# Performance work log

Measured on AMD Instinct MI355X. Metric: run time of the kernel, lower is better.

## Reference

```python
import jax, jax.numpy as jnp
import numpy as np

B, O, OBS, A, H = 512, 16, 128, 4, 64 * 8  # H=512
H = 512
LN_EPS = 1e-5


def _lin_init(key, fan_in, fan_out):
    k1, k2 = jax.random.split(key)
    lim = 1.0 / np.sqrt(fan_in)
    W = jax.random.uniform(k1, (fan_in, fan_out), jnp.float32, -lim, lim)
    b = jax.random.uniform(k2, (fan_out,), jnp.float32, -lim, lim)
    return W, b


def setup_inputs() -> dict:
    key = jax.random.key(0)
    ks = jax.random.split(key, 10)
    states = jax.random.normal(ks[0], (B, O, OBS), jnp.float32)
    action = jax.random.randint(ks[1], (B,), 0, A * O, jnp.int64)
    eW1, eb1 = _lin_init(ks[2], 2 * OBS, H)
    eW2, eb2 = _lin_init(ks[3], H, H)
    eW3, eb3 = _lin_init(ks[4], H, H)
    nW1, nb1 = _lin_init(ks[5], H + OBS + A, H)
    nW2, nb2 = _lin_init(ks[6], H, H)
    nW3, nb3 = _lin_init(ks[7], H, OBS)
    return dict(states=states, action=action,
                eW1=eW1, eb1=eb1, eW2=eW2, eb2=eb2,
                eg=jnp.ones((H,), jnp.float32), ebeta=jnp.zeros((H,), jnp.float32),
                eW3=eW3, eb3=eb3,
                nW1=nW1, nb1=nb1, nW2=nW2, nb2=nb2,
                ng=jnp.ones((H,), jnp.float32), nbeta=jnp.zeros((H,), jnp.float32),
                nW3=nW3, nb3=nb3)


def _ln(x, g, b):
    mu = jnp.mean(x, axis=-1, keepdims=True)
    var = jnp.mean((x - mu) ** 2, axis=-1, keepdims=True)
    return (x - mu) * jax.lax.rsqrt(var + LN_EPS) * g + b


def _mlp(x, W1, b1, W2, b2, g, beta, W3, b3):
    h = jax.nn.relu(x @ W1 + b1)
    h = jax.nn.relu(_ln(h @ W2 + b2, g, beta))
    return h @ W3 + b3


def _edge_index():
    # torch nonzero order: (i, j) for i in range(O), j != i; then batch offsets
    i = jnp.arange(O)[:, None]                   # [O,1]
    k = jnp.arange(O - 1)[None, :]               # [1,O-1]
    j = k + (k >= i)                             # skip self-loop
    row_l = jnp.broadcast_to(i, (O, O - 1)).reshape(-1)
    col_l = j.reshape(-1)
    off = (jnp.arange(B) * O)[:, None]           # [B,1]
    row = (row_l[None, :] + off).reshape(-1)     # [B*O*(O-1)]
    col = (col_l[None, :] + off).reshape(-1)
    return row, col


def reference(states, action, eW1, eb1, eW2, eb2, eg, ebeta, eW3, eb3,
              nW1, nb1, nW2, nb2, ng, nbeta, nW3, nb3):
    nodes = states.reshape(B * O, OBS)
    row, col = _edge_index()
    # edge model: gather pairs -> MLP
    e_in = jnp.concatenate([nodes[row], nodes[col]], axis=1)    # [E, 2*OBS]
    edge_attr = _mlp(e_in, eW1, eb1, eW2, eb2, eg, ebeta, eW3, eb3)  # [E, H]
    # action: one-hot over A*O, reshaped per-node
    act_vec = jax.nn.one_hot(action, A * O, dtype=states.dtype).reshape(B * O, A)
    node_in = jnp.concatenate([nodes, act_vec], axis=1)         # [B*O, OBS+A]
    # scatter: unsorted segment sum over source index (row)
    agg = jax.ops.segment_sum(edge_attr, row, num_segments=B * O)  # [B*O, H]
    node_in = jnp.concatenate([node_in, agg], axis=1)           # [B*O, OBS+A+H]
    out = _mlp(node_in, nW1, nb1, nW2, nb2, ng, nbeta, nW3, nb3)
    return out.reshape(B, O, OBS)
```

## Files before the change

kernel.cpp:

```cpp
#include <hip/hip_runtime.h>
#include <hip/hip_bf16.h>


using bf16 = __hip_bfloat16;
typedef __attribute__((ext_vector_type(8))) short bf16x8;
typedef __attribute__((ext_vector_type(4))) short short4v;
typedef __attribute__((ext_vector_type(4))) float f32x4;

#define LDK 40
#define LDQ 1032
#define LDN 520
#define LDT 72

#define SEG_EW1 32768
#define SEG_EW2 65536
#define SEG_EW3 65536
#define SEG_NW1 82432
#define SEG_NW2 65536
#define SEG_NW3 16384
#define SEG_EB3 128
#define SEG_NB1 128
#define SEG_TOT (SEG_EW1+SEG_EW2+SEG_EW3+SEG_NW1+SEG_NW2+SEG_NW3+SEG_EB3+SEG_NB1)

__device__ int g_valid = 0;
__device__ __align__(16) float g_wcopy[SEG_TOT * 4];
__device__ __align__(16) short g_eW1f[131072];
__device__ __align__(16) short g_eW2f[262144];
__device__ __align__(16) short g_nW1nf[65536];
__device__ __align__(16) short g_nW2f[262144];
__device__ __align__(16) short g_nW3f[65536];
__device__ __align__(16) short g_Wcf[262144];
__device__ __align__(16) float g_bfold[512];

__device__ __forceinline__ short f2bf(float f) {
  bf16 h = __float2bfloat16(f);
  return *reinterpret_cast<short*>(&h);
}
__device__ __forceinline__ float bs2f(short s) {
  bf16 h = *reinterpret_cast<bf16*>(&s);
  return __bfloat162float(h);
}
__device__ __forceinline__ f32x4 mfma16(bf16x8 a, bf16x8 b, f32x4 c) {
  return __builtin_amdgcn_mfma_f32_16x16x32_bf16(a, b, c, 0, 0, 0);
}
__device__ __forceinline__ bf16x8 ld8f(const float* p) {
  float4 a = *(const float4*)p;
  float4 b = *(const float4*)(p + 4);
  bf16x8 o;
  o[0] = f2bf(a.x); o[1] = f2bf(a.y); o[2] = f2bf(a.z); o[3] = f2bf(a.w);
  o[4] = f2bf(b.x); o[5] = f2bf(b.y); o[6] = f2bf(b.z); o[7] = f2bf(b.w);
  return o;
}
__device__ __forceinline__ void lgkm0_barrier() {
  asm volatile("s_waitcnt lgkmcnt(0)" ::: "memory");
  __builtin_amdgcn_s_barrier();
  asm volatile("" ::: "memory");
}

__global__ __launch_bounds__(256) void wcheck(
    const float* __restrict__ eW1, const float* __restrict__ eW2,
    const float* __restrict__ eW3, const float* __restrict__ nW1,
    const float* __restrict__ nW2, const float* __restrict__ nW3,
    const float* __restrict__ eb3, const float* __restrict__ nb1) {
  const int nt = gridDim.x * 256;
  const int tid = blockIdx.x * 256 + threadIdx.x;
  bool dirty = false;
#pragma unroll
  for (int k = 0; k < 4; ++k) {
    int idx = k * nt + tid;
    if (idx >= SEG_TOT) break;
    int i = idx;
    const uint4* src;
    if (i < SEG_EW1) src = (const uint4*)eW1 + i;
    else if ((i -= SEG_EW1) < SEG_EW2) src = (const uint4*)eW2 + i;
    else if ((i -= SEG_EW2) < SEG_EW3) src = (const uint4*)eW3 + i;
    else if ((i -= SEG_EW3) < SEG_NW1) src = (const uint4*)nW1 + i;
    else if ((i -= SEG_NW1) < SEG_NW2) src = (const uint4*)nW2 + i;
    else if ((i -= SEG_NW2) < SEG_NW3) src = (const uint4*)nW3 + i;
    else if ((i -= SEG_NW3) < SEG_EB3) src = (const uint4*)eb3 + i;
    else { i -= SEG_EB3; src = (const uint4*)nb1 + i; }
    uint4 a = *src;
    uint4* cp = (uint4*)g_wcopy + idx;
    uint4 b = *cp;
    if (a.x != b.x || a.y != b.y || a.z != b.z || a.w != b.w) {
      *cp = a;
      dirty = true;
    }
  }
  if (dirty) g_valid = 0;
}

__global__ __launch_bounds__(256) void mega_prep(
    const float* __restrict__ eW3, short* __restrict__ eW3b,
    const float* __restrict__ nW1, unsigned short* __restrict__ nW1at,
    const float* __restrict__ eW1, const float* __restrict__ eW2,
    const float* __restrict__ nW2, const float* __restrict__ nW3) {
  if (g_valid) return;
  __shared__ unsigned short ttile[32][33];
  __shared__ short ftile[32 * LDT];
  const int z = blockIdx.z, bx = blockIdx.x, t = threadIdx.x;
  if (z == 0) {
    if (bx >= 256) return;
    int i = (bx * 256 + t) * 4;
    float4 v = *(const float4*)(eW3 + i);
    short4v o;
    o.x = f2bf(v.x); o.y = f2bf(v.y); o.z = f2bf(v.z); o.w = f2bf(v.w);
    *(short4v*)(eW3b + i) = o;
    return;
  }
  if (z == 1) {
    if (bx >= 256) return;
    const float* src = nW1 + 132 * 512;
    int bc = (bx & 15) * 32, br = (bx >> 4) * 32;
    int tx = t & 31, ty = t >> 5;
    for (int i = ty; i < 32; i += 8) {
      short s = f2bf(src[(size_t)(br + i) * 512 + bc + tx]);
      ttile[i][tx] = *reinterpret_cast<unsigned short*>(&s);
    }
    __syncthreads();
    for (int i = ty; i < 32; i += 8)
      nW1at[(size_t)(bc + i) * 512 + br + tx] = ttile[tx][i];
    return;
  }
  const float* W;
  short* out;
  int ldw, kts, gq, goff, tot_sh;
  switch (z) {
    case 2: W = eW1;           out = g_eW1f;  ldw = 512; kts = 4;  gq = 8; goff = 0;  tot_sh = 6; break;
    case 3: W = eW1 + 128*512; out = g_eW1f;  ldw = 512; kts = 4;  gq = 8; goff = 32; tot_sh = 6; break;
    case 4: W = eW2;           out = g_eW2f;  ldw = 512; kts = 16; gq = 8; goff = 0;  tot_sh = 5; break;
    case 5: W = nW1;           out = g_nW1nf; ldw = 512; kts = 4;  gq = 8; goff = 0;  tot_sh = 5; break;
    case 6: W = nW2;           out = g_nW2f;  ldw = 512; kts = 16; gq = 8; goff = 0;  tot_sh = 5; break;
    default: W = nW3;          out = g_nW3f;  ldw = 128; kts = 16; gq = 2; goff = 0;  tot_sh = 3; break;
  }
  if (bx >= kts * gq) return;
  const int kt = bx / gq, qg = bx % gq;
  {
    int r = t >> 3, c0 = (t & 7) * 8;
    const float* src = W + (size_t)(kt * 32 + r) * ldw + qg * 64 + c0;
    *(bf16x8*)&ftile[r * LDT + c0] = ld8f(src);
  }
  __syncthreads();
  {
    int og = t >> 6, lane = t & 63, q = lane >> 4, lc = lane & 15;
    int gg = qg * 4 + og;
    size_t base = ((size_t)((kt << tot_sh) + gg + goff)) << 9;
    bf16x8 v;
#pragma unroll
    for (int j = 0; j < 8; ++j) v[j] = ftile[(q * 8 + j) * LDT + og * 16 + lc];
    *(bf16x8*)(out + base + lane * 8) = v;
  }
}

__global__ __launch_bounds__(256) void combo96(
    const bf16* __restrict__ nW1at, const bf16* __restrict__ eW3b,
    const float* __restrict__ eb3, const float* __restrict__ nb1,
    const float* __restrict__ nW1) {
  if (g_valid) return;
  __shared__ short Al[64 * LDK];
  __shared__ short Bl[64 * LDK];
  __shared__ float red[256];
  const int bid = blockIdx.x;
  const int t = threadIdx.x;
  const int wid = t >> 6, lane = t & 63, q = lane >> 4, lc = lane & 15;
  const f32x4 zz = {0.f, 0.f, 0.f, 0.f};

  if (bid < 64) {
    const int wm = wid >> 1, wn = wid & 1;
    const int n0 = (bid >> 3) * 64, k0 = (bid & 7) * 64;
    f32x4 acc[2][2];
#pragma unroll
    for (int mb = 0; mb < 2; ++mb)
#pragma unroll
      for (int nb = 0; nb < 2; ++nb) acc[mb][nb] = zz;
    const int sr = t >> 2, seg = t & 3;
    for (int h0 = 0; h0 < 512; h0 += 32) {
      *(uint4*)&Al[sr * LDK + seg * 8] =
          *(const uint4*)(nW1at + (size_t)(n0 + sr) * 512 + h0 + seg * 8);
      *(uint4*)&Bl[sr * LDK + seg * 8] =
          *(const uint4*)(eW3b + (size_t)(k0 + sr) * 512 + h0 + seg * 8);
      __syncthreads();
      bf16x8 af[2], bfr[2];
#pragma unroll
      for (int mb = 0; mb < 2; ++mb)
        af[mb] = *(const bf16x8*)&Al[(wm * 32 + mb * 16 + lc) * LDK + q * 8];
#pragma unroll
      for (int nb = 0; nb < 2; ++nb)
        bfr[nb] = *(const bf16x8*)&Bl[(wn * 32 + nb * 16 + lc) * LDK + q * 8];
#pragma unroll
      for (int mb = 0; mb < 2; ++mb)
#pragma unroll
        for (int nb = 0; nb < 2; ++nb)
          acc[mb][nb] = mfma16(af[mb], bfr[nb], acc[mb][nb]);
      __syncthreads();
    }
#pragma unroll
    for (int mb = 0; mb < 2; ++mb)
#pragma unroll
      for (int nb = 0; nb < 2; ++nb)
#pragma unroll
        for (int r = 0; r < 4; ++r) {
          int n = n0 + wm * 32 + mb * 16 + q * 4 + r;
          int k = k0 + wn * 32 + nb * 16 + lc;
          int kt = k >> 5, kin = k & 31, qf = kin >> 3, jf = kin & 7;
          g_Wcf[(((size_t)kt * 32 + (n >> 4)) * 64 + qf * 16 + (n & 15)) * 8 +
                jf] = f2bf(acc[mb][nb][r]);
        }
    return;
  }
  {
    const int n = (bid - 64) * 16 + (t & 15);
    const int sl = t >> 4;
    float s = 0.f;
#pragma unroll 8
    for (int h = sl * 32; h < sl * 32 + 32; ++h)
      s += eb3[h] * nW1[(size_t)(132 + h) * 512 + n];
    red[sl * 16 + (t & 15)] = s;
    __syncthreads();
    if (t < 16) {
      float tot = 0.f;
#pragma unroll
      for (int k = 0; k < 16; ++k) tot += red[k * 16 + t];
      g_bfold[(bid - 64) * 16 + t] = nb1[(bid - 64) * 16 + t] + 15.f * tot;
    }
  }
}

__global__ __launch_bounds__(512, 4) void mega(
    const float* __restrict__ states, const int* __restrict__ action,
    const float* __restrict__ eb1, const float* __restrict__ eb2,
    const float* __restrict__ eg, const float* __restrict__ ebt,
    const float* __restrict__ nW1, const float* __restrict__ nb2,
    const float* __restrict__ ng, const float* __restrict__ nbt,
    const float* __restrict__ nb3, float* __restrict__ Out) {
  __shared__ __align__(16) char smem[71168];
  short* PQL = (short*)(smem);
  short* sts = (short*)(smem + 33024);
  short* AbS = (short*)(smem + 33024);
  float* s_sum = (float*)(smem + 49408);
  float* s_sq = (float*)(smem + 51712);
  float* mr = (float*)(smem + 54016);
  short* SL = (short*)(smem + 54528);
  short* n1s = PQL;

  const bf16* const eW1f = (const bf16*)g_eW1f;
  const bf16* const eW2f = (const bf16*)g_eW2f;
  const bf16* const nW1nf = (const bf16*)g_nW1nf;
  const bf16* const nW2f = (const bf16*)g_nW2f;
  const bf16* const nW3f = (const bf16*)g_nW3f;
  const bf16* const Wcf = (const bf16*)g_Wcf;
  const float* const bfold = g_bfold;

  const int t = threadIdx.x;
  const int w = t >> 6, lane = t & 63, q = lane >> 4, lc = lane & 15;
  const int bb = blockIdx.x;

  if (bb == 0 && t == 0) g_valid = 1;

  if (t < 256) {
    int r = t >> 4, c8 = (t & 15) * 8;
    *(bf16x8*)&sts[r * 136 + c8] =
        ld8f(states + ((size_t)bb * 16 + r) * 128 + c8);
  }
  __syncthreads();

  {
    f32x4 acc[8];
#pragma unroll
    for (int nb = 0; nb < 8; ++nb) {
      int col = w * 128 + nb * 16 + lc;
      float bv = (col < 512) ? eb1[col] : 0.f;
      acc[nb] = {bv, bv, bv, bv};
    }
#pragma unroll
    for (int kt = 0; kt < 4; ++kt) {
      bf16x8 af = *(const bf16x8*)&sts[lc * 136 + kt * 32 + q * 8];
#pragma unroll
      for (int nb = 0; nb < 8; ++nb) {
        bf16x8 bfr = *(const bf16x8*)(eW1f +
                                      (((size_t)kt * 64 + w * 8 + nb) * 64 +
                                       lane) * 8);
        acc[nb] = mfma16(af, bfr, acc[nb]);
      }
    }
#pragma unroll
    for (int nb = 0; nb < 8; ++nb) {
      int col = w * 128 + nb * 16 + lc;
#pragma unroll
      for (int r = 0; r < 4; ++r)
        PQL[(q * 4 + r) * LDQ + col] = f2bf(acc[nb][r]);
    }
  }
  __syncthreads();

  const int ar = t >> 3;
  const int j8 = t & 7;
  const int gA = ar >> 4;
  const int slot = ar & 15;
  const bool padA = (slot == 15);
  const int wu = j8 ^ (ar & 7);
  const int aoff0 = lc * 64 + ((q ^ (lc & 7)) * 8);
  const int aoff1 = lc * 64 + (((4 + q) ^ (lc & 7)) * 8);
  const bf16* const eW2w = eW2f + (size_t)(w * 4) * 512 + lane * 8;
  short* const wdst0 = AbS + ar * 64 + wu * 8;

#pragma unroll 1
  for (int sg = 0; sg < 4; ++sg) {
    const int srcb = sg * 4 + gA;
    const int dstb = padA ? 0 : slot + (slot >= srcb ? 1 : 0);
    const short* pA = PQL + srcb * LDQ + j8 * 8;
    const short* qA = PQL + dstb * LDQ + 512 + j8 * 8;

    auto build = [&](int ks, int buf) {
      bf16x8 av = {0, 0, 0, 0, 0, 0, 0, 0};
      if (!padA) {
        bf16x8 pv = *(const bf16x8*)(pA + ks * 64);
        bf16x8 qv = *(const bf16x8*)(qA + ks * 64);
#pragma unroll
        for (int e = 0; e < 8; ++e)
          av[e] = f2bf(fmaxf(bs2f(pv[e]) + bs2f(qv[e]), 0.f));
      }
      *(bf16x8*)(wdst0 + buf * 4096) = av;
    };

    f32x4 acc[4][4];
#pragma unroll
    for (int nb = 0; nb < 4; ++nb) {
      float bv = eb2[w * 64 + nb * 16 + lc];
#pragma unroll
      for (int mb = 0; mb < 4; ++mb) acc[mb][nb] = {bv, bv, bv, bv};
    }

    build(0, 0);
    lgkm0_barrier();

#pragma unroll 1
    for (int ks = 0; ks < 8; ++ks) {
      const int cur = ks & 1;
      const short* Abc = AbS + cur * 4096;
      const bf16* bks = eW2w + (size_t)ks * 32768;
      bf16x8 a0[4], b0[4];
#pragma unroll
      for (int mb = 0; mb < 4; ++mb)
        a0[mb] = *(const bf16x8*)&Abc[mb * 1024 + aoff0];
#pragma unroll
      for (int nb = 0; nb < 4; ++nb)
        b0[nb] = *(const bf16x8*)(bks + nb * 512);
      __builtin_amdgcn_s_setprio(1);
#pragma unroll
      for (int mb = 0; mb < 4; ++mb)
#pragma unroll
        for (int nb = 0; nb < 4; ++nb)
          acc[mb][nb] = mfma16(a0[mb], b0[nb], acc[mb][nb]);
      __builtin_amdgcn_s_setprio(0);
      bf16x8 a1[4], b1[4];
#pragma unroll
      for (int nb = 0; nb < 4; ++nb)
        b1[nb] = *(const bf16x8*)(bks + 16384 + nb * 512);
#pragma unroll
      for (int mb = 0; mb < 4; ++mb)
        a1[mb] = *(const bf16x8*)&Abc[mb * 1024 + aoff1];
      if (ks < 7) build(ks + 1, cur ^ 1);
      __builtin_amdgcn_s_setprio(1);
#pragma unroll
      for (int mb = 0; mb < 4; ++mb)
#pragma unroll
        for (int nb = 0; nb < 4; ++nb)
          acc[mb][nb] = mfma16(a1[mb], b1[nb], acc[mb][nb]);
      __builtin_amdgcn_s_setprio(0);
      lgkm0_barrier();
    }

    float gv[4], bev[4];
#pragma unroll
    for (int nb = 0; nb < 4; ++nb) {
      int col = w * 64 + nb * 16 + lc;
      gv[nb] = eg[col];
      bev[nb] = ebt[col];
    }
#pragma unroll
    for (int mb = 0; mb < 4; ++mb) {
      float ps[4] = {0, 0, 0, 0}, pq2[4] = {0, 0, 0, 0};
#pragma unroll
      for (int nb = 0; nb < 4; ++nb)
#pragma unroll
        for (int r = 0; r < 4; ++r) {
          float x = acc[mb][nb][r];
          ps[r] += x;
          pq2[r] += x * x;
        }
#pragma unroll
      for (int d = 1; d < 16; d <<= 1)
#pragma unroll
        for (int r = 0; r < 4; ++r) {
          ps[r] += __shfl_xor(ps[r], d, 64);
          pq2[r] += __shfl_xor(pq2[r], d, 64);
        }
      if (lc == 0)
#pragma unroll
        for (int r = 0; r < 4; ++r) {
          int row = mb * 16 + q * 4 + r;
          s_sum[row * 9 + w] = ps[r];
          s_sq[row * 9 + w] = pq2[r];
        }
    }
    __syncthreads();
    if (t < 64) {
      float tot = 0.f, tsq = 0.f;
#pragma unroll
      for (int wv = 0; wv < 8; ++wv) {
        tot += s_sum[t * 9 + wv];
        tsq += s_sq[t * 9 + wv];
      }
      float m = tot * (1.f / 512.f);
      mr[t * 2] = m;
      mr[t * 2 + 1] = rsqrtf(tsq * (1.f / 512.f) - m * m + 1e-5f);
    }
    __syncthreads();
#pragma unroll
    for (int mb = 0; mb < 4; ++mb) {
      float sv[4] = {0, 0, 0, 0};
#pragma unroll
      for (int r = 0; r < 4; ++r) {
        int row = mb * 16 + q * 4 + r;
        float m = mr[row * 2], rstd = mr[row * 2 + 1];
#pragma unroll
        for (int nb = 0; nb < 4; ++nb) {
          float h = (acc[mb][nb][r] - m) * rstd * gv[nb] + bev[nb];
          h = fmaxf(h, 0.f);
          if (q * 4 + r != 15) sv[nb] += h;
        }
      }
#pragma unroll
      for (int nb = 0; nb < 4; ++nb) {
        sv[nb] += __shfl_xor(sv[nb], 16, 64);
        sv[nb] += __shfl_xor(sv[nb], 32, 64);
      }
      if (lane < 16)
#pragma unroll
        for (int nb = 0; nb < 4; ++nb)
          SL[(sg * 4 + mb) * LDN + w * 64 + nb * 16 + lc] = f2bf(sv[nb]);
    }
  }
  __syncthreads();

  if (t < 256) {
    int r = t >> 4, c8 = (t & 15) * 8;
    *(bf16x8*)&sts[r * 136 + c8] =
        ld8f(states + ((size_t)bb * 16 + r) * 128 + c8);
  }
  __syncthreads();

  {
    f32x4 acc[4];
#pragma unroll
    for (int nb = 0; nb < 4; ++nb) {
      float bv = bfold[w * 64 + nb * 16 + lc];
      acc[nb] = {bv, bv, bv, bv};
    }
#pragma unroll
    for (int kt = 0; kt < 4; ++kt) {
      bf16x8 af = *(const bf16x8*)&sts[lc * 136 + kt * 32 + q * 8];
#pragma unroll
      for (int nb = 0; nb < 4; ++nb) {
        bf16x8 bfr = *(const bf16x8*)(nW1nf +
                                      (((size_t)kt * 32 + w * 4 + nb) * 64 +
                                       lane) * 8);
        acc[nb] = mfma16(af, bfr, acc[nb]);
      }
    }
#pragma unroll 2
    for (int kt = 0; kt < 16; ++kt) {
      bf16x8 af = *(const bf16x8*)&SL[lc * LDN + kt * 32 + q * 8];
#pragma unroll
      for (int nb = 0; nb < 4; ++nb) {
        bf16x8 bfr = *(const bf16x8*)(Wcf +
                                      (((size_t)kt * 32 + w * 4 + nb) * 64 +
                                       lane) * 8);
        acc[nb] = mfma16(af, bfr, acc[nb]);
      }
    }
    int a = action[bb];
    int aw = a >> 2, ac4 = a & 3;
#pragma unroll
    for (int nb = 0; nb < 4; ++nb) {
      int col = w * 64 + nb * 16 + lc;
      float awv = nW1[(size_t)(128 + ac4) * 512 + col];
#pragma unroll
      for (int r = 0; r < 4; ++r) {
        int row = q * 4 + r;
        float x = acc[nb][r] + (row == aw ? awv : 0.f);
        n1s[row * LDN + col] = f2bf(fmaxf(x, 0.f));
      }
    }
  }
  __syncthreads();

  {
    f32x4 acc[4];
#pragma unroll
    for (int nb = 0; nb < 4; ++nb) {
      float bv = nb2[w * 64 + nb * 16 + lc];
      acc[nb] = {bv, bv, bv, bv};
    }
#pragma unroll 2
    for (int kt = 0; kt < 16; ++kt) {
      bf16x8 af = *(const bf16x8*)&n1s[lc * LDN + kt * 32 + q * 8];
#pragma unroll
      for (int nb = 0; nb < 4; ++nb) {
        bf16x8 bfr = *(const bf16x8*)(nW2f +
                                      (((size_t)kt * 32 + w * 4 + nb) * 64 +
                                       lane) * 8);
        acc[nb] = mfma16(af, bfr, acc[nb]);
      }
    }
    float gv[4], bev[4];
    float ps[4] = {0, 0, 0, 0}, pq2[4] = {0, 0, 0, 0};
#pragma unroll
    for (int nb = 0; nb < 4; ++nb) {
      int col = w * 64 + nb * 16 + lc;
      gv[nb] = ng[col];
      bev[nb] = nbt[col];
#pragma unroll
      for (int r = 0; r < 4; ++r) {
        ps[r] += acc[nb][r];
        pq2[r] += acc[nb][r] * acc[nb][r];
      }
    }
#pragma unroll
    for (int d = 1; d < 16; d <<= 1)
#pragma unroll
      for (int r = 0; r < 4; ++r) {
        ps[r] += __shfl_xor(ps[r], d, 64);
        pq2[r] += __shfl_xor(pq2[r], d, 64);
      }
    if (lc == 0)
#pragma unroll
      for (int r = 0; r < 4; ++r) {
        s_sum[(q * 4 + r) * 9 + w] = ps[r];
        s_sq[(q * 4 + r) * 9 + w] = pq2[r];
      }
    __syncthreads();
    if (t < 16) {
      float tot = 0.f, tsq = 0.f;
#pragma unroll
      for (int wv = 0; wv < 8; ++wv) {
        tot += s_sum[t * 9 + wv];
        tsq += s_sq[t * 9 + wv];
      }
      float m = tot * (1.f / 512.f);
      mr[t * 2] = m;
      mr[t * 2 + 1] = rsqrtf(tsq * (1.f / 512.f) - m * m + 1e-5f);
    }
    __syncthreads();
#pragma unroll
    for (int r = 0; r < 4; ++r) {
      int row = q * 4 + r;
      float m = mr[row * 2], rstd = mr[row * 2 + 1];
#pragma unroll
      for (int nb = 0; nb < 4; ++nb) {
        int col = w * 64 + nb * 16 + lc;
        float h = (acc[nb][r] - m) * rstd * gv[nb] + bev[nb];
        n1s[row * LDN + col] = f2bf(fmaxf(h, 0.f));
      }
    }
  }
  __syncthreads();

  {
    float b3 = nb3[w * 16 + lc];
    f32x4 acc3 = {b3, b3, b3, b3};
#pragma unroll 2
    for (int kt = 0; kt < 16; ++kt) {
      bf16x8 af = *(const bf16x8*)&n1s[lc * LDN + kt * 32 + q * 8];
      bf16x8 bfr = *(const bf16x8*)(nW3f +
                                    (((size_t)kt * 8 + w) * 64 + lane) * 8);
      acc3 = mfma16(af, bfr, acc3);
    }
    int col = w * 16 + lc;
#pragma unroll
    for (int r = 0; r < 4; ++r)
      Out[((size_t)bb * 16 + q * 4 + r) * 128 + col] = acc3[r];
  }
}

extern "C" void kernel_launch(void* const* d_in, const int* in_sizes, int n_in,
                              void* d_out, int out_size, void* d_ws,
                              size_t ws_size, hipStream_t stream) {
  const float* states = (const float*)d_in[0];
  const int* action = (const int*)d_in[1];
  const float* eW1 = (const float*)d_in[2];
  const float* eb1 = (const float*)d_in[3];
  const float* eW2 = (const float*)d_in[4];
  const float* eb2 = (const float*)d_in[5];
  const float* eg = (const float*)d_in[6];
  const float* ebt = (const float*)d_in[7];
  const float* eW3 = (const float*)d_in[8];
  const float* eb3 = (const float*)d_in[9];
  const float* nW1 = (const float*)d_in[10];
  const float* nb1 = (const float*)d_in[11];
  const float* nW2 = (const float*)d_in[12];
  const float* nb2 = (const float*)d_in[13];
  const float* ng = (const float*)d_in[14];
  const float* nbt = (const float*)d_in[15];
  const float* nW3 = (const float*)d_in[16];
  const float* nb3 = (const float*)d_in[17];

  char* w = (char*)d_ws;
  bf16* eW3b = (bf16*)w;   w += (size_t)262144 * 2;
  bf16* nW1at = (bf16*)w;  w += (size_t)262144 * 2;

  wcheck<<<328, 256, 0, stream>>>(eW1, eW2, eW3, nW1, nW2, nW3, eb3, nb1);

  mega_prep<<<dim3(256, 1, 8), 256, 0, stream>>>(
      eW3, (short*)eW3b, nW1, (unsigned short*)nW1at, eW1, eW2, nW2, nW3);

  combo96<<<96, 256, 0, stream>>>(nW1at, eW3b, eb3, nb1, nW1);

  mega<<<512, 512, 0, stream>>>(states, action, eb1, eb2, eg, ebt, nW1, nb2,
                                ng, nbt, nb3, (float*)d_out);

  (void)in_sizes; (void)n_in; (void)out_size; (void)ws_size;
}
```

Baseline: 222.2 us.

## Swizzle shared layouts and quad-buffer edge A tiles with cross-segment prefetch

Replaces padded LDS strides with XOR-swizzled layouts for the P/Q table, SL and n1s buffers, so bank conflicts are avoided without padding. The eW2 k-loop is restructured into pairs of k-steps over four A buffers, building two steps ahead. The next segment's first tiles are prefetched during the current segment's last pair, which removes the per-segment prologue barrier. It adds LDS footprint (81920 bytes) and a syncthreads per segment, which may lower occupancy.

```diff
diff --git a/kernel.cpp b/kernel.cpp
--- a/kernel.cpp
+++ b/kernel.cpp
@@ -8,8 +8,6 @@
 typedef __attribute__((ext_vector_type(4))) float f32x4;
 
 #define LDK 40
-#define LDQ 1032
-#define LDN 520
 #define LDT 72
 
 #define SEG_EW1 32768
@@ -233,14 +231,14 @@
     const float* __restrict__ nW1, const float* __restrict__ nb2,
     const float* __restrict__ ng, const float* __restrict__ nbt,
     const float* __restrict__ nb3, float* __restrict__ Out) {
-  __shared__ __align__(16) char smem[71168];
+  __shared__ __align__(16) char smem[81920];
   short* PQL = (short*)(smem);
-  short* sts = (short*)(smem + 33024);
-  short* AbS = (short*)(smem + 33024);
-  float* s_sum = (float*)(smem + 49408);
-  float* s_sq = (float*)(smem + 51712);
-  float* mr = (float*)(smem + 54016);
-  short* SL = (short*)(smem + 54528);
+  short* sts = (short*)(smem + 32768);
+  short* AbS = (short*)(smem + 32768);
+  float* s_sum = (float*)(smem + 49152);
+  float* s_sq = (float*)(smem + 51456);
+  float* mr = (float*)(smem + 53760);
+  short* SL = (short*)(smem + 65536);
   short* n1s = PQL;
 
   const bf16* const eW1f = (const bf16*)g_eW1f;
@@ -254,6 +252,8 @@
   const int t = threadIdx.x;
   const int w = t >> 6, lane = t & 63, q = lane >> 4, lc = lane & 15;
   const int bb = blockIdx.x;
+  const int xb = (lc >> 2) & 1;
+  const int q2 = q ^ (lc & 3);
 
   if (bb == 0 && t == 0) g_valid = 1;
 
@@ -265,12 +265,12 @@
   __syncthreads();
 
   {
-    f32x4 acc[8];
+    f32x4 acc1[8];
 #pragma unroll
     for (int nb = 0; nb < 8; ++nb) {
       int col = w * 128 + nb * 16 + lc;
       float bv = (col < 512) ? eb1[col] : 0.f;
-      acc[nb] = {bv, bv, bv, bv};
+      acc1[nb] = {bv, bv, bv, bv};
     }
 #pragma unroll
     for (int kt = 0; kt < 4; ++kt) {
@@ -280,15 +280,18 @@
         bf16x8 bfr = *(const bf16x8*)(eW1f +
                                       (((size_t)kt * 64 + w * 8 + nb) * 64 +
                                        lane) * 8);
-        acc[nb] = mfma16(af, bfr, acc[nb]);
+        acc1[nb] = mfma16(af, bfr, acc1[nb]);
       }
     }
 #pragma unroll
     for (int nb = 0; nb < 8; ++nb) {
       int col = w * 128 + nb * 16 + lc;
-#pragma unroll
-      for (int r = 0; r < 4; ++r)
-        PQL[(q * 4 + r) * LDQ + col] = f2bf(acc[nb][r]);
+      int u = col >> 3, lo = col & 7;
+#pragma unroll
+      for (int r = 0; r < 4; ++r) {
+        int row = q * 4 + r;
+        PQL[row * 1024 + (((u ^ (row & 7)) << 3) | lo)] = f2bf(acc1[nb][r]);
+      }
     }
   }
   __syncthreads();
@@ -304,25 +307,32 @@
   const bf16* const eW2w = eW2f + (size_t)(w * 4) * 512 + lane * 8;
   short* const wdst0 = AbS + ar * 64 + wu * 8;
 
+  auto setPtrs = [&](int sg, const short*& pp, const short*& qq) {
+    int srcb = sg * 4 + gA;
+    int dstb = padA ? 0 : slot + (slot >= srcb ? 1 : 0);
+    pp = PQL + srcb * 1024 + (j8 ^ (srcb & 7)) * 8;
+    qq = PQL + dstb * 1024 + 512 + (j8 ^ (dstb & 7)) * 8;
+  };
+  auto build = [&](const short* pp, const short* qq, int ks, int buf) {
+    bf16x8 av = {0, 0, 0, 0, 0, 0, 0, 0};
+    if (!padA) {
+      bf16x8 pv = *(const bf16x8*)(pp + ks * 64);
+      bf16x8 qv = *(const bf16x8*)(qq + ks * 64);
+#pragma unroll
+      for (int e = 0; e < 8; ++e)
+        av[e] = f2bf(fmaxf(bs2f(pv[e]) + bs2f(qv[e]), 0.f));
+    }
+    *(bf16x8*)(wdst0 + buf * 4096) = av;
+  };
+
+  const short *pA, *qA;
+  setPtrs(0, pA, qA);
+  build(pA, qA, 0, 0);
+  build(pA, qA, 1, 1);
+  lgkm0_barrier();
+
 #pragma unroll 1
   for (int sg = 0; sg < 4; ++sg) {
-    const int srcb = sg * 4 + gA;
-    const int dstb = padA ? 0 : slot + (slot >= srcb ? 1 : 0);
-    const short* pA = PQL + srcb * LDQ + j8 * 8;
-    const short* qA = PQL + dstb * LDQ + 512 + j8 * 8;
-
-    auto build = [&](int ks, int buf) {
-      bf16x8 av = {0, 0, 0, 0, 0, 0, 0, 0};
-      if (!padA) {
-        bf16x8 pv = *(const bf16x8*)(pA + ks * 64);
-        bf16x8 qv = *(const bf16x8*)(qA + ks * 64);
-#pragma unroll
-        for (int e = 0; e < 8; ++e)
-          av[e] = f2bf(fmaxf(bs2f(pv[e]) + bs2f(qv[e]), 0.f));
-      }
-      *(bf16x8*)(wdst0 + buf * 4096) = av;
-    };
-
     f32x4 acc[4][4];
 #pragma unroll
     for (int nb = 0; nb < 4; ++nb) {
@@ -331,44 +341,73 @@
       for (int mb = 0; mb < 4; ++mb) acc[mb][nb] = {bv, bv, bv, bv};
     }
 
-    build(0, 0);
-    lgkm0_barrier();
-
-#pragma unroll 1
-    for (int ks = 0; ks < 8; ++ks) {
-      const int cur = ks & 1;
-      const short* Abc = AbS + cur * 4096;
-      const bf16* bks = eW2w + (size_t)ks * 32768;
-      bf16x8 a0[4], b0[4];
+    auto ks_pair = [&](int ks0, bool bld, const short* bp, const short* bq,
+                       int bs0, int bb0, int bs1, int bb1) {
+      const short* A0 = AbS + (ks0 & 3) * 4096;
+      const short* A1 = AbS + ((ks0 + 1) & 3) * 4096;
+      const bf16* bk0 = eW2w + (size_t)ks0 * 32768;
+      const bf16* bk1 = bk0 + 32768;
+      bf16x8 a[4], b[4];
+#pragma unroll
+      for (int mb = 0; mb < 4; ++mb) a[mb] = *(const bf16x8*)&A0[mb * 1024 + aoff0];
+#pragma unroll
+      for (int nb = 0; nb < 4; ++nb) b[nb] = *(const bf16x8*)(bk0 + nb * 512);
+      __builtin_amdgcn_s_setprio(1);
 #pragma unroll
       for (int mb = 0; mb < 4; ++mb)
-        a0[mb] = *(const bf16x8*)&Abc[mb * 1024 + aoff0];
-#pragma unroll
-      for (int nb = 0; nb < 4; ++nb)
-        b0[nb] = *(const bf16x8*)(bks + nb * 512);
+#pragma unroll
+        for (int nb = 0; nb < 4; ++nb)
+          acc[mb][nb] = mfma16(a[mb], b[nb], acc[mb][nb]);
+      __builtin_amdgcn_s_setprio(0);
+#pragma unroll
+      for (int nb = 0; nb < 4; ++nb) b[nb] = *(const bf16x8*)(bk0 + 16384 + nb * 512);
+#pragma unroll
+      for (int mb = 0; mb < 4; ++mb) a[mb] = *(const bf16x8*)&A0[mb * 1024 + aoff1];
+      if (bld) build(bp, bq, bs0, bb0);
       __builtin_amdgcn_s_setprio(1);
 #pragma unroll
       for (int mb = 0; mb < 4; ++mb)
 #pragma unroll
         for (int nb = 0; nb < 4; ++nb)
-          acc[mb][nb] = mfma16(a0[mb], b0[nb], acc[mb][nb]);
+          acc[mb][nb] = mfma16(a[mb], b[nb], acc[mb][nb]);
       __builtin_amdgcn_s_setprio(0);
-      bf16x8 a1[4], b1[4];
-#pragma unroll
-      for (int nb = 0; nb < 4; ++nb)
-        b1[nb] = *(const bf16x8*)(bks + 16384 + nb * 512);
+#pragma unroll
+      for (int mb = 0; mb < 4; ++mb) a[mb] = *(const bf16x8*)&A1[mb * 1024 + aoff0];
+#pragma unroll
+      for (int nb = 0; nb < 4; ++nb) b[nb] = *(const bf16x8*)(bk1 + nb * 512);
+      __builtin_amdgcn_s_setprio(1);
 #pragma unroll
       for (int mb = 0; mb < 4; ++mb)
-        a1[mb] = *(const bf16x8*)&Abc[mb * 1024 + aoff1];
-      if (ks < 7) build(ks + 1, cur ^ 1);
+#pragma unroll
+        for (int nb = 0; nb < 4; ++nb)
+          acc[mb][nb] = mfma16(a[mb], b[nb], acc[mb][nb]);
+      __builtin_amdgcn_s_setprio(0);
+#pragma unroll
+      for (int nb = 0; nb < 4; ++nb) b[nb] = *(const bf16x8*)(bk1 + 16384 + nb * 512);
+#pragma unroll
+      for (int mb = 0; mb < 4; ++mb) a[mb] = *(const bf16x8*)&A1[mb * 1024 + aoff1];
+      if (bld) build(bp, bq, bs1, bb1);
       __builtin_amdgcn_s_setprio(1);
 #pragma unroll
       for (int mb = 0; mb < 4; ++mb)
 #pragma unroll
         for (int nb = 0; nb < 4; ++nb)
-          acc[mb][nb] = mfma16(a1[mb], b1[nb], acc[mb][nb]);
+          acc[mb][nb] = mfma16(a[mb], b[nb], acc[mb][nb]);
       __builtin_amdgcn_s_setprio(0);
       lgkm0_barrier();
+    };
+
+#pragma unroll 1
+    for (int iv = 0; iv < 3; ++iv)
+      ks_pair(2 * iv, true, pA, qA,
+              2 * iv + 2, (2 * iv + 2) & 3, 2 * iv + 3, (2 * iv + 3) & 3);
+    if (sg < 3) {
+      const short *pN, *qN;
+      setPtrs(sg + 1, pN, qN);
+      ks_pair(6, true, pN, qN, 0, 0, 1, 1);
+      pA = pN; qA = qN;
+    } else {
+      ks_pair(6, false, pA, qA, 0, 0, 0, 0);
     }
 
     float gv[4], bev[4];
@@ -436,13 +475,17 @@
         sv[nb] += __shfl_xor(sv[nb], 16, 64);
         sv[nb] += __shfl_xor(sv[nb], 32, 64);
       }
-      if (lane < 16)
-#pragma unroll
-        for (int nb = 0; nb < 4; ++nb)
-          SL[(sg * 4 + mb) * LDN + w * 64 + nb * 16 + lc] = f2bf(sv[nb]);
-    }
-  }
-  __syncthreads();
+      if (lane < 16) {
+        int row = sg * 4 + mb;
+#pragma unroll
+        for (int nb = 0; nb < 4; ++nb) {
+          int u = w * 8 + nb * 2 + (lane >> 3);
+          SL[row * 512 + (((u ^ (row & 7)) << 3) | (lane & 7))] = f2bf(sv[nb]);
+        }
+      }
+    }
+    __syncthreads();
+  }
 
   if (t < 256) {
     int r = t >> 4, c8 = (t & 15) * 8;
@@ -471,7 +514,7 @@
     }
 #pragma unroll 2
     for (int kt = 0; kt < 16; ++kt) {
-      bf16x8 af = *(const bf16x8*)&SL[lc * LDN + kt * 32 + q * 8];
+      bf16x8 af = *(const bf16x8*)&SL[lc * 512 + ((kt ^ xb) * 32 + q2 * 8)];
 #pragma unroll
       for (int nb = 0; nb < 4; ++nb) {
         bf16x8 bfr = *(const bf16x8*)(Wcf +
@@ -486,11 +529,12 @@
     for (int nb = 0; nb < 4; ++nb) {
       int col = w * 64 + nb * 16 + lc;
       float awv = nW1[(size_t)(128 + ac4) * 512 + col];
+      int u = col >> 3, lo = col & 7;
 #pragma unroll
       for (int r = 0; r < 4; ++r) {
         int row = q * 4 + r;
         float x = acc[nb][r] + (row == aw ? awv : 0.f);
-        n1s[row * LDN + col] = f2bf(fmaxf(x, 0.f));
+        n1s[row * 1024 + (((u ^ (row & 7)) << 3) | lo)] = f2bf(fmaxf(x, 0.f));
       }
     }
   }
@@ -505,7 +549,7 @@
     }
 #pragma unroll 2
     for (int kt = 0; kt < 16; ++kt) {
-      bf16x8 af = *(const bf16x8*)&n1s[lc * LDN + kt * 32 + q * 8];
+      bf16x8 af = *(const bf16x8*)&n1s[lc * 1024 + ((kt ^ xb) * 32 + q2 * 8)];
 #pragma unroll
       for (int nb = 0; nb < 4; ++nb) {
         bf16x8 bfr = *(const bf16x8*)(nW2f +
@@ -515,7 +559,7 @@
       }
     }
     float gv[4], bev[4];
-    float ps[4] = {0, 0, 0, 0}, pq2[4] = {0, 0, 0, 0};
+    float ps[4] = {0, 0, 0, 0}, pq2v[4] = {0, 0, 0, 0};
 #pragma unroll
     for (int nb = 0; nb < 4; ++nb) {
       int col = w * 64 + nb * 16 + lc;
@@ -524,7 +568,7 @@
 #pragma unroll
       for (int r = 0; r < 4; ++r) {
         ps[r] += acc[nb][r];
-        pq2[r] += acc[nb][r] * acc[nb][r];
+        pq2v[r] += acc[nb][r] * acc[nb][r];
       }
     }
 #pragma unroll
@@ -532,13 +576,13 @@
 #pragma unroll
       for (int r = 0; r < 4; ++r) {
         ps[r] += __shfl_xor(ps[r], d, 64);
-        pq2[r] += __shfl_xor(pq2[r], d, 64);
+        pq2v[r] += __shfl_xor(pq2v[r], d, 64);
       }
     if (lc == 0)
 #pragma unroll
       for (int r = 0; r < 4; ++r) {
         s_sum[(q * 4 + r) * 9 + w] = ps[r];
-        s_sq[(q * 4 + r) * 9 + w] = pq2[r];
+        s_sq[(q * 4 + r) * 9 + w] = pq2v[r];
       }
     __syncthreads();
     if (t < 16) {
@@ -561,7 +605,8 @@
       for (int nb = 0; nb < 4; ++nb) {
         int col = w * 64 + nb * 16 + lc;
         float h = (acc[nb][r] - m) * rstd * gv[nb] + bev[nb];
-        n1s[row * LDN + col] = f2bf(fmaxf(h, 0.f));
+        int u = col >> 3, lo = col & 7;
+        n1s[row * 1024 + (((u ^ (row & 7)) << 3) | lo)] = f2bf(fmaxf(h, 0.f));
       }
     }
   }
@@ -572,7 +617,7 @@
     f32x4 acc3 = {b3, b3, b3, b3};
 #pragma unroll 2
     for (int kt = 0; kt < 16; ++kt) {
-      bf16x8 af = *(const bf16x8*)&n1s[lc * LDN + kt * 32 + q * 8];
+      bf16x8 af = *(const bf16x8*)&n1s[lc * 1024 + ((kt ^ xb) * 32 + q2 * 8)];
       bf16x8 bfr = *(const bf16x8*)(nW3f +
                                     (((size_t)kt * 8 + w) * 64 + lane) * 8);
       acc3 = mfma16(af, bfr, acc3);
```

Result: slower. 410.3 us (+84.7%).
